# Optimization experiments

Measured on AMD Instinct MI355X. Metric: run time of the kernel, lower is better.

## Reference

```python
import jax, jax.numpy as jnp
import numpy as np
from jax import lax

A = 3          # anchors per scale
C = 80         # num foreground classes (COCO)
NMS_THRESH = 0.45
NMS_TOPK = 400
POST_NMS = 100


def setup_inputs() -> dict:
    key = jax.random.key(0)
    k0, k1, k2 = jax.random.split(key, 3)
    B = 8
    ch = A * (C + 5)  # 255
    # raw head outputs (pre-decode conv activations), modest scale so exp() stays sane
    tip0 = jax.random.normal(k0, (B, ch, 19, 19), jnp.float32) * 0.5
    tip1 = jax.random.normal(k1, (B, ch, 38, 38), jnp.float32) * 0.5
    tip2 = jax.random.normal(k2, (B, ch, 76, 76), jnp.float32) * 0.5
    # standard YOLOv3 COCO anchors, deepest scale (stride 32) first
    anchors0 = jnp.array([[116., 90.], [156., 198.], [373., 326.]], jnp.float32)
    anchors1 = jnp.array([[30., 61.], [62., 45.], [59., 119.]], jnp.float32)
    anchors2 = jnp.array([[10., 13.], [16., 30.], [33., 23.]], jnp.float32)
    return dict(tip0=tip0, tip1=tip1, tip2=tip2,
                anchors0=anchors0, anchors1=anchors1, anchors2=anchors2)


def _decode(tip, anchors, stride):
    """YOLOOutputV3 inference decode. tip: (B, A*(C+5), H, W)."""
    B, _, H, W = tip.shape
    # (B, A*(C+5), H*W) -> (B, H*W, A, C+5)
    pred = tip.reshape(B, A * (C + 5), H * W).transpose(0, 2, 1).reshape(B, H * W, A, C + 5)
    gx, gy = jnp.meshgrid(jnp.arange(W), jnp.arange(H))       # each (H, W)
    offsets = jnp.stack([gx, gy], -1).reshape(1, H * W, 1, 2).astype(tip.dtype)
    centers = (jax.nn.sigmoid(pred[..., :2]) + offsets) * stride          # (B,HW,A,2)
    scales = jnp.exp(pred[..., 2:4]) * anchors.reshape(1, 1, A, 2)        # (B,HW,A,2)
    conf = jax.nn.sigmoid(pred[..., 4:5])                                 # objectness
    cls_scores = jax.nn.sigmoid(pred[..., 5:]) * conf                      # (B,HW,A,C)
    wh = scales * 0.5
    bbox = jnp.concatenate([centers - wh, centers + wh], -1)               # corner format
    return bbox.reshape(B, H * W * A, 4), cls_scores.reshape(B, H * W * A, C)


def _pairwise_iou(b):
    """b: (K,4) corner boxes -> (K,K) IoU."""
    x1, y1, x2, y2 = b[:, 0], b[:, 1], b[:, 2], b[:, 3]
    area = jnp.maximum(x2 - x1, 0.) * jnp.maximum(y2 - y1, 0.)
    iw = jnp.maximum(jnp.minimum(x2[:, None], x2[None, :]) - jnp.maximum(x1[:, None], x1[None, :]), 0.)
    ih = jnp.maximum(jnp.minimum(y2[:, None], y2[None, :]) - jnp.maximum(y1[:, None], y1[None, :]), 0.)
    inter = iw * ih
    return inter / (area[:, None] + area[None, :] - inter + 1e-12)


def _nms_single(det):
    """Class-aware greedy NMS on one image. det: (M,6) = (cid, score, x1,y1,x2,y2)."""
    K = NMS_TOPK
    _, idx = lax.top_k(det[:, 1], K)     # sort by score, keep top K
    d = det[idx]                          # (K,6), descending score
    iou = _pairwise_iou(d[:, 2:6])
    same = d[:, 0][:, None] == d[:, 0][None, :]   # only same class suppresses
    valid = d[:, 1] > 0.
    rng = jnp.arange(K)

    def body(i, keep):
        sup = (iou[i] > NMS_THRESH) & same[i] & (rng > i) & keep[i] & valid[i]
        return keep & ~sup

    keep = lax.fori_loop(0, K, body, jnp.ones((K,), bool)) & valid
    d = jnp.where(keep[:, None], d, jnp.full_like(d, -1.))
    order = jnp.argsort(-d[:, 1])         # kept (sorted) first, suppressed (-1) last
    return d[order][:POST_NMS]            # (POST_NMS, 6)


def _detect(tip0, tip1, tip2, anchors0, anchors1, anchors2):
    dets = []
    for tip, anc, stride in ((tip0, anchors0, 32), (tip1, anchors1, 16), (tip2, anchors2, 8)):
        bbox, scores = _decode(tip, anc, stride)          # (B,N,4), (B,N,C)
        B, N, _ = bbox.shape
        ids = jnp.broadcast_to(jnp.arange(C, dtype=bbox.dtype)[None, None, :, None], (B, N, C, 1))
        sc = scores[..., None]                            # (B,N,C,1)
        bx = jnp.broadcast_to(bbox[:, :, None, :], (B, N, C, 4))
        dets.append(jnp.concatenate([ids, sc, bx], -1).reshape(B, N * C, 6))
    det = jnp.concatenate(dets, 1)                        # (B, M, 6)
    return jax.vmap(_nms_single)(det)                     # (B, POST_NMS, 6)


def reference(tip0, tip1, tip2, anchors0, anchors1, anchors2):
    res = _detect(tip0, tip1, tip2, anchors0, anchors1, anchors2)
    ids = res[..., 0:1]
    scores = res[..., 1:2]
    bboxes = res[..., 2:6]
    return ids, scores, bboxes
```

## Files before the change

### kernel.cpp

```cpp
#include <hip/hip_runtime.h>
#include <stdint.h>

#define NUMA 3
#define NUMC 80
#define CAP  49152
#define KTOP 400
#define POST 100
#define EQCAP 1024
#define PFCAP 2048
#define KEY0 0x3EE66666u
#define KEYTOP 0x3F800000u
#define LBUF 1024
#define NMASK (KTOP * 7)
#define CPB 20

typedef float f32x4 __attribute__((ext_vector_type(4)));

__device__ __forceinline__ float sigmoidf_(float x) { return 1.0f / (1.0f + expf(-x)); }
__device__ __forceinline__ unsigned uminu(unsigned a, unsigned b) { return a < b ? a : b; }

__device__ __forceinline__ float thr_for(float cf) {
    if (!(cf >= 0.45f)) return 3.0e38f;
    float q = 0.449f / cf;
    float r = q / (1.0f - q);
    return logf(r) - 0.01f;
}

__global__ __launch_bounds__(256) void score_main(
        const float* __restrict__ t0, const float* __restrict__ t1,
        const float* __restrict__ t2,
        unsigned* __restrict__ ccnt, unsigned* __restrict__ ckey,
        unsigned* __restrict__ cidx)
{
    __shared__ unsigned lkey[LBUF], lidx[LBUF];
    __shared__ unsigned lcnt, lbase;
    const int tid = threadIdx.x;
    if (tid == 0) lcnt = 0;
    __syncthreads();

    const int ba = blockIdx.z;
    const int b = ba / 3, a = ba - 3 * b;
    const int c0 = blockIdx.y * CPB;
    const int cx = blockIdx.x;

    #define LEMIT(SC, IDX) do { \
        unsigned key_ = __float_as_uint(SC); \
        if (key_ >= KEY0) { \
            unsigned pos_ = atomicAdd(&lcnt, 1u); \
            if (pos_ < LBUF) { lkey[pos_] = key_; lidx[pos_] = (IDX); } \
        } \
    } while (0)

    if (cx < 2) {
        const int hw = cx * 256 + tid;
        if (hw < 361) {
            const float* base = t0 + (size_t)(b * 255 + a * 85) * 361;
            float cr = base[4 * 361 + hw];
            const float* p0 = base + (size_t)(5 + c0) * 361 + hw;
            float xv[CPB];
            #pragma unroll
            for (int u = 0; u < CPB; u++) xv[u] = p0[u * 361];
            float cf = sigmoidf_(cr);
            float xt = thr_for(cf);
            unsigned ib = (unsigned)((hw * NUMA + a) * NUMC + c0);
            #pragma unroll
            for (int u = 0; u < CPB; u++)
                if (xv[u] > xt) LEMIT(sigmoidf_(xv[u]) * cf, ib + (unsigned)u);
        }
    } else {
        const float* tip; int vHW, v, candOff;
        if (cx < 4) { tip = t1; vHW = 361;  v = (cx - 2) * 256 + tid; candOff = 86640; }
        else        { tip = t2; vHW = 1444; v = (cx - 4) * 256 + tid; candOff = 433200; }
        if (v < vHW) {
            const f32x4* bp = (const f32x4*)(tip + (size_t)(b * 255 + a * 85) * (size_t)(vHW * 4));
            f32x4 cv = bp[(size_t)4 * vHW + v];
            const f32x4* p0 = bp + (size_t)(5 + c0) * vHW + v;
            f32x4 sv[CPB];
            #pragma unroll
            for (int u = 0; u < CPB; u++) sv[u] = p0[(size_t)u * vHW];
            float cf0 = sigmoidf_(cv[0]), cf1 = sigmoidf_(cv[1]);
            float cf2 = sigmoidf_(cv[2]), cf3 = sigmoidf_(cv[3]);
            float xt0 = thr_for(cf0), xt1 = thr_for(cf1);
            float xt2 = thr_for(cf2), xt3 = thr_for(cf3);
            unsigned ib0 = (unsigned)(candOff + (v * 4 * NUMA + a) * NUMC + c0);
            #pragma unroll
            for (int u = 0; u < CPB; u++) {
                unsigned ib = ib0 + (unsigned)u;
                if (sv[u][0] > xt0) LEMIT(sigmoidf_(sv[u][0]) * cf0, ib);
                if (sv[u][1] > xt1) LEMIT(sigmoidf_(sv[u][1]) * cf1, ib + 240);
                if (sv[u][2] > xt2) LEMIT(sigmoidf_(sv[u][2]) * cf2, ib + 480);
                if (sv[u][3] > xt3) LEMIT(sigmoidf_(sv[u][3]) * cf3, ib + 720);
            }
        }
    }
    #undef LEMIT

    __syncthreads();
    if (tid == 0) {
        unsigned c = lcnt;
        if (c > LBUF) {
            atomicOr(&ccnt[b], 0x80000000u);
            lbase = 0xFFFFFFFFu;
        } else {
            lbase = atomicAdd(&ccnt[b], c);
        }
    }
    __syncthreads();
    unsigned c = uminu(lcnt, (unsigned)LBUF);
    unsigned basep = lbase;
    if (basep != 0xFFFFFFFFu) {
        for (unsigned i = tid; i < c; i += 256) {
            unsigned p = basep + i;
            if (p < CAP) {
                ckey[(size_t)b * CAP + p] = lkey[i];
                cidx[(size_t)b * CAP + p] = lidx[i];
            }
        }
    }
}

__device__ __forceinline__ void wave_select(const unsigned* h, int nbins, unsigned rank,
                                            unsigned* resv, int tid)
{
    if (tid >= 64) return;
    const int lane = tid;
    const int cs = nbins >> 6;
    unsigned v = 0;
    for (int k = 0; k < cs; k++) {
        int off = (k + lane) & (cs - 1);
        v += h[lane * cs + off];
    }
    unsigned S = v;
    #pragma unroll
    for (int o = 1; o < 64; o <<= 1) {
        unsigned t = (unsigned)__shfl_down((int)S, o);
        if (lane + o < 64) S += t;
    }
    unsigned long long bm = __ballot(S >= rank);
    if (bm == 0ull) bm = 1ull;
    int C = 63 - __builtin_clzll(bm);
    unsigned SC = (unsigned)__builtin_amdgcn_readlane((int)S, C);
    unsigned vC = (unsigned)__builtin_amdgcn_readlane((int)v, C);
    unsigned rem = rank - (SC - vC);
    unsigned w = (lane < cs) ? h[C * cs + lane] : 0u;
    unsigned T = w;
    #pragma unroll
    for (int o = 1; o < 64; o <<= 1) {
        unsigned t = (unsigned)__shfl_down((int)T, o);
        if (lane + o < 64) T += t;
    }
    unsigned long long bm2 = __ballot((T >= rem) && (lane < cs));
    if (bm2 == 0ull) bm2 = 1ull;
    int B = 63 - __builtin_clzll(bm2);
    unsigned TB = (unsigned)__builtin_amdgcn_readlane((int)T, B);
    unsigned wB = (unsigned)__builtin_amdgcn_readlane((int)w, B);
    if (lane == 0) {
        resv[0] = (unsigned)(C * cs + B);
        resv[1] = rem - (TB - wB);
    }
}

__global__ __launch_bounds__(1024) void topk_sel(
        const float* __restrict__ t0, const float* __restrict__ t1,
        const float* __restrict__ t2,
        const float* __restrict__ anc0, const float* __restrict__ anc1,
        const float* __restrict__ anc2,
        const unsigned* __restrict__ ccnt,
        unsigned* __restrict__ ckey, unsigned* __restrict__ cidx,
        float* __restrict__ dX1, float* __restrict__ dY1,
        float* __restrict__ dX2, float* __restrict__ dY2,
        float* __restrict__ dSC, unsigned* __restrict__ dCID)
{
    const int b = blockIdx.x;
    const int tid = threadIdx.x;
    const int T = 1024;

    __shared__ unsigned hist[4096];
    __shared__ unsigned resv[2];
    __shared__ unsigned selk[512], seli[512];
    __shared__ unsigned eqi[EQCAP];
    __shared__ unsigned pk[PFCAP], pi[PFCAP];
    __shared__ unsigned cnts[3];
    __shared__ unsigned fcnt;

    unsigned* ck = ckey + (size_t)b * CAP;
    unsigned* ci = cidx + (size_t)b * CAP;
    unsigned nraw = ccnt[b];
    unsigned kbase = KEY0;

    bool cold = !(nraw >= KTOP && nraw <= CAP);
    if (cold) {
        const int NPOS = 3 * (361 + 1444 + 5776);
        for (int i = tid; i < 2048; i += T) hist[i] = 0;
        if (tid == 0) fcnt = 0;
        __syncthreads();
        for (int p = tid; p < NPOS; p += T) {
            const float* tip; int HW, pp;
            if (p < 1083)      { tip = t0; HW = 361;  pp = p; }
            else if (p < 5415) { tip = t1; HW = 1444; pp = p - 1083; }
            else               { tip = t2; HW = 5776; pp = p - 5415; }
            int a = pp / HW, hwl = pp - a * HW;
            const float* base = tip + (size_t)(b * 255 + a * 85) * HW;
            float cf = sigmoidf_(base[4 * HW + hwl]);
            for (int u = 0; u < NUMC; u++) {
                float sc = sigmoidf_(base[(size_t)(5 + u) * HW + hwl]) * cf;
                atomicAdd(&hist[__float_as_uint(sc) >> 19], 1u);
            }
        }
        __syncthreads();
        wave_select(hist, 2048, KTOP, resv, tid);
        __syncthreads();
        unsigned cutkey = resv[0] << 19;
        __syncthreads();
        for (int p = tid; p < NPOS; p += T) {
            const float* tip; int HW, pp, candOff;
            if (p < 1083)      { tip = t0; HW = 361;  pp = p;        candOff = 0; }
            else if (p < 5415) { tip = t1; HW = 1444; pp = p - 1083; candOff = 86640; }
            else               { tip = t2; HW = 5776; pp = p - 5415; candOff = 433200; }
            int a = pp / HW, hwl = pp - a * HW;
            const float* base = tip + (size_t)(b * 255 + a * 85) * HW;
            float cf = sigmoidf_(base[4 * HW + hwl]);
            unsigned ib0 = (unsigned)(candOff + (hwl * NUMA + a) * NUMC);
            for (int u = 0; u < NUMC; u++) {
                float sc = sigmoidf_(base[(size_t)(5 + u) * HW + hwl]) * cf;
                unsigned key = __float_as_uint(sc);
                if (key >= cutkey) {
                    unsigned pos = atomicAdd(&fcnt, 1u);
                    if (pos < CAP) { ck[pos] = key; ci[pos] = ib0 + (unsigned)u; }
                }
            }
        }
        __syncthreads();
        nraw = fcnt;
        kbase = cutkey;
    }
    unsigned n = uminu(nraw, (unsigned)CAP);

    unsigned span = (KEYTOP - kbase) + 1u;
    unsigned SH = 0;
    while ((span >> SH) > 2047u) SH++;

    for (int i = tid; i < 2048; i += T) hist[i] = 0;
    __syncthreads();
    {
        unsigned n4 = n >> 2;
        const uint4* ck4 = (const uint4*)ck;
        for (unsigned i = tid; i < n4; i += T) {
            uint4 k = ck4[i];
            atomicAdd(&hist[(k.x - kbase) >> SH], 1u);
            atomicAdd(&hist[(k.y - kbase) >> SH], 1u);
            atomicAdd(&hist[(k.z - kbase) >> SH], 1u);
            atomicAdd(&hist[(k.w - kbase) >> SH], 1u);
        }
        for (unsigned i = (n4 << 2) + tid; i < n; i += T)
            atomicAdd(&hist[(ck[i] - kbase) >> SH], 1u);
    }
    __syncthreads();
    wave_select(hist, 2048, KTOP, resv, tid);
    __syncthreads();
    unsigned Bf = resv[0];
    __syncthreads();

    if (tid == 0) { cnts[0] = 0; cnts[1] = 0; cnts[2] = 0; }
    __syncthreads();
    for (unsigned i = tid; i < n; i += T) {
        unsigned k = ck[i];
        if (((k - kbase) >> SH) >= Bf) {
            unsigned q = atomicAdd(&cnts[2], 1u);
            if (q < (unsigned)PFCAP) { pk[q] = k; pi[q] = ci[i]; }
        }
    }
    __syncthreads();
    unsigned pfCnt = cnts[2];
    bool useP = (pfCnt <= (unsigned)PFCAP);
    unsigned m = useP ? pfCnt : n;
    bool direct = useP && (pfCnt <= 512u);

    if (direct) {
        for (int i = tid; i < 512; i += T) { selk[i] = 0u; seli[i] = 0xFFFFFFFFu; }
        __syncthreads();
        for (unsigned i = tid; i < pfCnt; i += T) { selk[i] = pk[i]; seli[i] = pi[i]; }
        __syncthreads();
    } else {
        for (int i = tid; i < 4096; i += T) hist[i] = 0;
        __syncthreads();
        for (unsigned i = tid; i < m; i += T) {
            unsigned k = useP ? pk[i] : ck[i];
            atomicAdd(&hist[k >> 19], 1u);
        }
        __syncthreads();
        wave_select(hist, 4096, KTOP, resv, tid);
        __syncthreads();
        unsigned b1 = resv[0], r2 = resv[1];
        __syncthreads();

        for (int i = tid; i < 4096; i += T) hist[i] = 0;
        __syncthreads();
        for (unsigned i = tid; i < m; i += T) {
            unsigned k = useP ? pk[i] : ck[i];
            if ((k >> 19) == b1) atomicAdd(&hist[(k >> 7) & 0xFFFu], 1u);
        }
        __syncthreads();
        wave_select(hist, 4096, r2, resv, tid);
        __syncthreads();
        unsigned b2 = resv[0], r3 = resv[1];
        __syncthreads();

        for (int i = tid; i < 128; i += T) hist[i] = 0;
        __syncthreads();
        unsigned pref = (b1 << 12) | b2;
        for (unsigned i = tid; i < m; i += T) {
            unsigned k = useP ? pk[i] : ck[i];
            if ((k >> 7) == pref) atomicAdd(&hist[k & 127u], 1u);
        }
        __syncthreads();
        wave_select(hist, 128, r3, resv, tid);
        __syncthreads();
        unsigned b3 = resv[0], needEq = resv[1];
        unsigned K400 = (b1 << 19) | (b2 << 7) | b3;
        __syncthreads();

        for (int i = tid; i < 512; i += T) { selk[i] = 0u; seli[i] = 0xFFFFFFFFu; }
        for (int i = tid; i < EQCAP; i += T) eqi[i] = 0xFFFFFFFFu;
        __syncthreads();
        for (unsigned i = tid; i < m; i += T) {
            unsigned k = useP ? pk[i] : ck[i];
            if (k > K400) {
                unsigned idx = useP ? pi[i] : ci[i];
                unsigned p = atomicAdd(&cnts[0], 1u);
                if (p < 512u) { selk[p] = k; seli[p] = idx; }
            } else if (k == K400) {
                unsigned idx = useP ? pi[i] : ci[i];
                unsigned q = atomicAdd(&cnts[1], 1u);
                if (q < (unsigned)EQCAP) eqi[q] = idx;
            }
        }
        __syncthreads();
        unsigned selCnt = uminu(cnts[0], (unsigned)KTOP);
        unsigned eqN   = uminu(cnts[1], (unsigned)EQCAP);

        if (eqN > needEq) {
            int P2 = 1; while ((unsigned)P2 < eqN) P2 <<= 1;
            for (int k2 = 2; k2 <= P2; k2 <<= 1) {
                for (int j = k2 >> 1; j > 0; j >>= 1) {
                    __syncthreads();
                    for (int i = tid; i < P2; i += T) {
                        int ixj = i ^ j;
                        if (ixj > i && ixj < P2) {
                            unsigned va = eqi[i], vb = eqi[ixj];
                            bool up = ((i & k2) == 0);
                            if (up ? (va > vb) : (va < vb)) { eqi[i] = vb; eqi[ixj] = va; }
                        }
                    }
                }
            }
            __syncthreads();
        }
        for (unsigned t2v = tid; t2v < needEq; t2v += T) {
            unsigned p = selCnt + t2v;
            if (p < KTOP) { selk[p] = K400; seli[p] = eqi[t2v]; }
        }
        __syncthreads();
    }

    for (int k2 = 2; k2 <= 512; k2 <<= 1) {
        int j = k2 >> 1;
        for (; j >= 64; j >>= 1) {
            __syncthreads();
            if (tid < 512) {
                int i = tid, ixj = i ^ j;
                if (ixj > i) {
                    unsigned ka = selk[i], kb = selk[ixj], ia = seli[i], ib = seli[ixj];
                    bool before = (ka > kb) || (ka == kb && ia < ib);
                    bool up = ((i & k2) == 0);
                    if (up ? !before : before) {
                        selk[i] = kb; selk[ixj] = ka; seli[i] = ib; seli[ixj] = ia;
                    }
                }
            }
        }
        __syncthreads();
        if (tid < 512) {
            for (; j > 0; j >>= 1) {
                int i = tid, ixj = i ^ j;
                if (ixj > i) {
                    unsigned ka = selk[i], kb = selk[ixj], ia = seli[i], ib = seli[ixj];
                    bool before = (ka > kb) || (ka == kb && ia < ib);
                    bool up = ((i & k2) == 0);
                    if (up ? !before : before) {
                        selk[i] = kb; selk[ixj] = ka; seli[i] = ib; seli[ixj] = ia;
                    }
                }
            }
        }
    }
    __syncthreads();

    if (tid < KTOP) {
        unsigned idx = seli[tid];
        int o = b * KTOP + tid;
        if (idx == 0xFFFFFFFFu) {
            dX1[o] = -1.f; dY1[o] = -1.f; dX2[o] = -1.f; dY2[o] = -1.f;
            dSC[o] = __uint_as_float(selk[tid]); dCID[o] = 0u;
        } else {
            const float* tip; const float* anc; int HW, W, candOff; float strideF;
            if (idx < 86640u)       { tip = t0; anc = anc0; HW = 361;  W = 19; strideF = 32.f; candOff = 0; }
            else if (idx < 433200u) { tip = t1; anc = anc1; HW = 1444; W = 38; strideF = 16.f; candOff = 86640; }
            else                    { tip = t2; anc = anc2; HW = 5776; W = 76; strideF = 8.f;  candOff = 433200; }
            unsigned local = idx - (unsigned)candOff;
            int cls = (int)(local % NUMC);
            int nn  = (int)(local / NUMC);
            int a = nn % NUMA, hwl = nn / NUMA;
            const float* base = tip + (size_t)(b * 255 + a * 85) * HW + hwl;
            float tx = base[0];
            float ty = base[(size_t)HW];
            float tw = base[(size_t)2 * HW];
            float th = base[(size_t)3 * HW];
            float fx = (float)(hwl % W), fy = (float)(hwl / W);
            float cx = (sigmoidf_(tx) + fx) * strideF;
            float cy = (sigmoidf_(ty) + fy) * strideF;
            float hw_ = expf(tw) * anc[2 * a]     * 0.5f;
            float hh_ = expf(th) * anc[2 * a + 1] * 0.5f;
            dX1[o] = cx - hw_; dY1[o] = cy - hh_;
            dX2[o] = cx + hw_; dY2[o] = cy + hh_;
            dSC[o] = __uint_as_float(selk[tid]);
            dCID[o] = (unsigned)cls;
        }
    }
}

__global__ __launch_bounds__(256) void mask_kernel(
        const float* __restrict__ dX1, const float* __restrict__ dY1,
        const float* __restrict__ dX2, const float* __restrict__ dY2,
        const unsigned* __restrict__ dCID, unsigned long long* __restrict__ maskG)
{
    __shared__ float lx1[KTOP], ly1[KTOP], lx2[KTOP], ly2[KTOP];
    __shared__ int lcid[KTOP];
    const int b = blockIdx.y;
    const int tid = threadIdx.x;
    for (int i = tid; i < KTOP; i += 256) {
        int o = b * KTOP + i;
        lx1[i] = dX1[o]; ly1[i] = dY1[o];
        lx2[i] = dX2[o]; ly2[i] = dY2[o];
        lcid[i] = (int)dCID[o];
    }
    __syncthreads();
    int p = blockIdx.x * 256 + tid;
    if (p < NMASK) {
        int i = p / 7, w = p - i * 7;
        float x1i = lx1[i], y1i = ly1[i], x2i = lx2[i], y2i = ly2[i];
        float ai = fmaxf(x2i - x1i, 0.f) * fmaxf(y2i - y1i, 0.f);
        int cidI = lcid[i];
        unsigned long long m = 0ull;
        int j0 = w * 64;
        int rot = (9 * w) & 63;
        for (int t = 0; t < 64; t++) {
            int j = j0 + ((t + rot) & 63);
            if (j >= KTOP || j <= i) continue;
            if (lcid[j] != cidI) continue;
            float iw = fminf(x2i, lx2[j]) - fmaxf(x1i, lx1[j]);
            float ih = fminf(y2i, ly2[j]) - fmaxf(y1i, ly1[j]);
            iw = fmaxf(iw, 0.f); ih = fmaxf(ih, 0.f);
            float inter = iw * ih;
            float aj = fmaxf(lx2[j] - lx1[j], 0.f) * fmaxf(ly2[j] - ly1[j], 0.f);
            float iou = inter / (ai + aj - inter + 1e-12f);
            if (iou > 0.45f) m |= (1ull << (j - j0));
        }
        maskG[(size_t)b * NMASK + p] = m;
    }
}

__global__ __launch_bounds__(512) void greedy_kernel(
        const float* __restrict__ dX1, const float* __restrict__ dY1,
        const float* __restrict__ dX2, const float* __restrict__ dY2,
        const float* __restrict__ dSC, const unsigned* __restrict__ dCID,
        const unsigned long long* __restrict__ maskG, float* __restrict__ out)
{
    __shared__ unsigned long long maskL[NMASK];
    __shared__ unsigned long long vkeep[7];
    __shared__ float oid[POST], osc[POST], obb[POST * 4];
    const int b = blockIdx.x;
    const int tid = threadIdx.x;

    for (int i = tid; i < NMASK; i += 512) maskL[i] = maskG[(size_t)b * NMASK + i];
    if (tid < POST) { oid[tid] = -1.f; osc[tid] = -1.f; }
    if (tid < POST * 4) obb[tid] = -1.f;
    __syncthreads();

    if (tid < 64) {
        const int lane = tid;
        unsigned long long keep = 0ull;
        if (lane < 7) keep = (lane == 6) ? 0xFFFFull : ~0ull;
        unsigned long long mb[8];
        #pragma unroll
        for (int k = 0; k < 8; k++)
            mb[k] = (lane < 7) ? maskL[k * 7 + lane] : 0ull;
        for (int ib = 0; ib < KTOP; ib += 8) {
            #pragma unroll
            for (int k = 0; k < 8; k++) {
                int i = ib + k;
                unsigned long long m = mb[k];
                int nf = ib + 8 + k;
                mb[k] = (lane < 7 && nf < KTOP) ? maskL[nf * 7 + lane] : 0ull;
                int w = i >> 6;
                unsigned klo = (unsigned)__builtin_amdgcn_readlane((int)(unsigned)(keep & 0xFFFFFFFFull), w);
                unsigned khi = (unsigned)__builtin_amdgcn_readlane((int)(unsigned)(keep >> 32), w);
                unsigned long long kw = ((unsigned long long)khi << 32) | klo;
                if ((kw >> (i & 63)) & 1ull) keep &= ~m;
            }
        }
        if (lane < 7) vkeep[lane] = keep;
    }
    __syncthreads();

    if (tid < KTOP) {
        int w = tid >> 6, bp = tid & 63;
        unsigned long long kw = vkeep[w];
        if ((kw >> bp) & 1ull) {
            int r = 0;
            for (int q = 0; q < w; q++) r += __popcll(vkeep[q]);
            r += __popcll(kw & ((1ull << bp) - 1ull));
            if (r < POST) {
                int o = b * KTOP + tid;
                oid[r] = (float)(int)dCID[o];
                osc[r] = dSC[o];
                obb[r * 4 + 0] = dX1[o];
                obb[r * 4 + 1] = dY1[o];
                obb[r * 4 + 2] = dX2[o];
                obb[r * 4 + 3] = dY2[o];
            }
        }
    }
    __syncthreads();
    if (tid < POST) {
        out[b * POST + tid]       = oid[tid];
        out[800 + b * POST + tid] = osc[tid];
    }
    if (tid < POST * 4) out[1600 + b * POST * 4 + tid] = obb[tid];
}

extern "C" void kernel_launch(void* const* d_in, const int* in_sizes, int n_in,
                              void* d_out, int out_size, void* d_ws, size_t ws_size,
                              hipStream_t stream)
{
    const float* tip0 = (const float*)d_in[0];
    const float* tip1 = (const float*)d_in[1];
    const float* tip2 = (const float*)d_in[2];
    const float* anc0 = (const float*)d_in[3];
    const float* anc1 = (const float*)d_in[4];
    const float* anc2 = (const float*)d_in[5];
    float* out = (float*)d_out;

    unsigned* ccnt = (unsigned*)d_ws;
    unsigned* ckey = ccnt + 8;
    unsigned* cidx = ckey + (size_t)8 * CAP;
    float*    dX1  = (float*)(cidx + (size_t)8 * CAP);
    float*    dY1  = dX1 + 8 * KTOP;
    float*    dX2  = dY1 + 8 * KTOP;
    float*    dY2  = dX2 + 8 * KTOP;
    float*    dSC  = dY2 + 8 * KTOP;
    unsigned* dCID = (unsigned*)(dSC + 8 * KTOP);
    unsigned long long* maskG = (unsigned long long*)(dCID + 8 * KTOP);

    hipMemsetAsync(ccnt, 0, 8 * sizeof(unsigned), stream);

    dim3 g(10, 80 / CPB, 24);
    score_main<<<g, 256, 0, stream>>>(tip0, tip1, tip2, ccnt, ckey, cidx);
    topk_sel<<<8, 1024, 0, stream>>>(tip0, tip1, tip2, anc0, anc1, anc2,
                                     ccnt, ckey, cidx,
                                     dX1, dY1, dX2, dY2, dSC, dCID);
    mask_kernel<<<dim3((NMASK + 255) / 256, 8), 256, 0, stream>>>(
        dX1, dY1, dX2, dY2, dCID, maskG);
    greedy_kernel<<<8, 512, 0, stream>>>(dX1, dY1, dX2, dY2, dSC, dCID, maskG, out);
}
```

Baseline: 183.6 us.

## Fuse IoU mask and greedy NMS kernels via last-block-done atomic counter

Merges the mask and greedy NMS kernels into a single launch. Each block computes its slice of the suppression mask, then increments a per-batch atomic counter, and the last block to finish runs the greedy scan and writes the output. Box data is kept in shared memory so the gather skips the global reloads. This removes one kernel launch and its dependency gap, at the cost of higher shared-memory use per block and threadfence/atomic synchronisation.

```diff
diff --git a/kernel.cpp b/kernel.cpp
--- a/kernel.cpp
+++ b/kernel.cpp
@@ -13,6 +13,7 @@
 #define LBUF 1024
 #define NMASK (KTOP * 7)
 #define CPB 20
+#define MBLK 11
 
 typedef float f32x4 __attribute__((ext_vector_type(4)));
 
@@ -429,22 +430,30 @@
     }
 }
 
-__global__ __launch_bounds__(256) void mask_kernel(
+__global__ __launch_bounds__(256) void mask_greedy(
         const float* __restrict__ dX1, const float* __restrict__ dY1,
         const float* __restrict__ dX2, const float* __restrict__ dY2,
-        const unsigned* __restrict__ dCID, unsigned long long* __restrict__ maskG)
+        const float* __restrict__ dSC, const unsigned* __restrict__ dCID,
+        unsigned long long* __restrict__ maskG, unsigned* __restrict__ done,
+        float* __restrict__ out)
 {
-    __shared__ float lx1[KTOP], ly1[KTOP], lx2[KTOP], ly2[KTOP];
+    __shared__ float lx1[KTOP], ly1[KTOP], lx2[KTOP], ly2[KTOP], lsc[KTOP];
     __shared__ int lcid[KTOP];
+    __shared__ unsigned long long maskL[NMASK];
+    __shared__ unsigned long long vkeep[7];
+    __shared__ float oid[POST], osc[POST], obb[POST * 4];
+    __shared__ int lastFlag;
     const int b = blockIdx.y;
     const int tid = threadIdx.x;
+
     for (int i = tid; i < KTOP; i += 256) {
         int o = b * KTOP + i;
         lx1[i] = dX1[o]; ly1[i] = dY1[o];
         lx2[i] = dX2[o]; ly2[i] = dY2[o];
-        lcid[i] = (int)dCID[o];
-    }
-    __syncthreads();
+        lsc[i] = dSC[o]; lcid[i] = (int)dCID[o];
+    }
+    __syncthreads();
+
     int p = blockIdx.x * 256 + tid;
     if (p < NMASK) {
         int i = p / 7, w = p - i * 7;
@@ -468,23 +477,20 @@
         }
         maskG[(size_t)b * NMASK + p] = m;
     }
-}
-
-__global__ __launch_bounds__(512) void greedy_kernel(
-        const float* __restrict__ dX1, const float* __restrict__ dY1,
-        const float* __restrict__ dX2, const float* __restrict__ dY2,
-        const float* __restrict__ dSC, const unsigned* __restrict__ dCID,
-        const unsigned long long* __restrict__ maskG, float* __restrict__ out)
-{
-    __shared__ unsigned long long maskL[NMASK];
-    __shared__ unsigned long long vkeep[7];
-    __shared__ float oid[POST], osc[POST], obb[POST * 4];
-    const int b = blockIdx.x;
-    const int tid = threadIdx.x;
-
-    for (int i = tid; i < NMASK; i += 512) maskL[i] = maskG[(size_t)b * NMASK + i];
-    if (tid < POST) { oid[tid] = -1.f; osc[tid] = -1.f; }
-    if (tid < POST * 4) obb[tid] = -1.f;
+    __syncthreads();
+
+    __threadfence();
+    if (tid == 0) {
+        unsigned old = atomicAdd(&done[b], 1u);
+        lastFlag = (old == MBLK - 1) ? 1 : 0;
+    }
+    __syncthreads();
+    if (!lastFlag) return;
+    __threadfence();
+
+    for (int i = tid; i < NMASK; i += 256) maskL[i] = maskG[(size_t)b * NMASK + i];
+    for (int i = tid; i < POST; i += 256) { oid[i] = -1.f; osc[i] = -1.f; }
+    for (int i = tid; i < POST * 4; i += 256) obb[i] = -1.f;
     __syncthreads();
 
     if (tid < 64) {
@@ -513,30 +519,30 @@
     }
     __syncthreads();
 
-    if (tid < KTOP) {
-        int w = tid >> 6, bp = tid & 63;
+    for (int i = tid; i < KTOP; i += 256) {
+        int w = i >> 6, bp = i & 63;
         unsigned long long kw = vkeep[w];
         if ((kw >> bp) & 1ull) {
             int r = 0;
             for (int q = 0; q < w; q++) r += __popcll(vkeep[q]);
             r += __popcll(kw & ((1ull << bp) - 1ull));
             if (r < POST) {
-                int o = b * KTOP + tid;
-                oid[r] = (float)(int)dCID[o];
-                osc[r] = dSC[o];
-                obb[r * 4 + 0] = dX1[o];
-                obb[r * 4 + 1] = dY1[o];
-                obb[r * 4 + 2] = dX2[o];
-                obb[r * 4 + 3] = dY2[o];
-            }
-        }
-    }
-    __syncthreads();
-    if (tid < POST) {
-        out[b * POST + tid]       = oid[tid];
-        out[800 + b * POST + tid] = osc[tid];
-    }
-    if (tid < POST * 4) out[1600 + b * POST * 4 + tid] = obb[tid];
+                oid[r] = (float)lcid[i];
+                osc[r] = lsc[i];
+                obb[r * 4 + 0] = lx1[i];
+                obb[r * 4 + 1] = ly1[i];
+                obb[r * 4 + 2] = lx2[i];
+                obb[r * 4 + 3] = ly2[i];
+            }
+        }
+    }
+    __syncthreads();
+    for (int i = tid; i < POST; i += 256) {
+        out[b * POST + i]       = oid[i];
+        out[800 + b * POST + i] = osc[i];
+    }
+    for (int i = tid; i < POST * 4; i += 256)
+        out[1600 + b * POST * 4 + i] = obb[i];
 }
 
 extern "C" void kernel_launch(void* const* d_in, const int* in_sizes, int n_in,
@@ -552,7 +558,8 @@
     float* out = (float*)d_out;
 
     unsigned* ccnt = (unsigned*)d_ws;
-    unsigned* ckey = ccnt + 8;
+    unsigned* done = ccnt + 8;
+    unsigned* ckey = done + 8;
     unsigned* cidx = ckey + (size_t)8 * CAP;
     float*    dX1  = (float*)(cidx + (size_t)8 * CAP);
     float*    dY1  = dX1 + 8 * KTOP;
@@ -562,14 +569,13 @@
     unsigned* dCID = (unsigned*)(dSC + 8 * KTOP);
     unsigned long long* maskG = (unsigned long long*)(dCID + 8 * KTOP);
 
-    hipMemsetAsync(ccnt, 0, 8 * sizeof(unsigned), stream);
+    hipMemsetAsync(ccnt, 0, 16 * sizeof(unsigned), stream);
 
     dim3 g(10, 80 / CPB, 24);
     score_main<<<g, 256, 0, stream>>>(tip0, tip1, tip2, ccnt, ckey, cidx);
     topk_sel<<<8, 1024, 0, stream>>>(tip0, tip1, tip2, anc0, anc1, anc2,
                                      ccnt, ckey, cidx,
                                      dX1, dY1, dX2, dY2, dSC, dCID);
-    mask_kernel<<<dim3((NMASK + 255) / 256, 8), 256, 0, stream>>>(
-        dX1, dY1, dX2, dY2, dCID, maskG);
-    greedy_kernel<<<8, 512, 0, stream>>>(dX1, dY1, dX2, dY2, dSC, dCID, maskG, out);
+    mask_greedy<<<dim3(MBLK, 8), 256, 0, stream>>>(
+        dX1, dY1, dX2, dY2, dSC, dCID, maskG, done, out);
 }
```

After: 188.4 us. 1.03x slower.
